# Kernel tuning notes

Measured on AMD Instinct MI355X. Metric: run time of the kernel, lower is better.

## Reference

```python
import jax, jax.numpy as jnp
import numpy as np

NEG = -1e30   # finite stand-in for -inf (keeps vjp NaN-free)
BLANK = 0


def _ctc_loss_mean(logits, targets):
    """CTC loss matching torch.nn.CTCLoss(blank=0, zero_infinity=True,
    reduction='mean') applied to log_softmax(logits).permute(1,0,2), with
    input_lengths = T and uniform target_lengths = L.

    logits:  (B, T, K) raw scores
    targets: (B, L) int labels in [1, K) (no blanks)
    """
    B, T, K = logits.shape
    L = targets.shape[1]
    S = 2 * L + 1  # extended label sequence: blank-interleaved

    logp = jax.nn.log_softmax(logits, axis=-1)  # (B, T, K)

    # extended labels ext = [blank, y1, blank, y2, ..., yL, blank]
    ext = jnp.full((B, S), BLANK, dtype=targets.dtype)
    ext = ext.at[:, 1::2].set(targets)  # (B, S)

    # per-step log-probs of extended labels: lp[b, t, s] = logp[b, t, ext[b, s]]
    lp = jnp.take_along_axis(logp, ext[:, None, :], axis=2)  # (B, T, S)

    # skip transition (s-2 -> s) allowed iff ext[s] != blank and ext[s] != ext[s-2]
    skip = jnp.concatenate(
        [jnp.zeros((B, 2), dtype=bool),
         (ext[:, 2:] != BLANK) & (ext[:, 2:] != ext[:, :-2])], axis=1)  # (B, S)

    # alpha init at t = 0
    alpha0 = jnp.full((B, S), NEG, dtype=logp.dtype)
    alpha0 = alpha0.at[:, 0].set(lp[:, 0, 0]).at[:, 1].set(lp[:, 0, 1])

    pad1 = jnp.full((B, 1), NEG, dtype=logp.dtype)
    pad2 = jnp.full((B, 2), NEG, dtype=logp.dtype)

    def step(alpha, lp_t):
        a1 = alpha                                            # stay
        a2 = jnp.concatenate([pad1, alpha[:, :-1]], axis=1)   # advance 1
        a3 = jnp.concatenate([pad2, alpha[:, :-2]], axis=1)   # advance 2
        a3 = jnp.where(skip, a3, NEG)
        new = jnp.logaddexp(jnp.logaddexp(a1, a2), a3) + lp_t
        return new, None

    xs = jnp.swapaxes(lp[:, 1:, :], 0, 1)  # (T-1, B, S)
    alpha, _ = jax.lax.scan(step, alpha0, xs)

    # total log-likelihood: end at last blank or last label
    logl = jnp.logaddexp(alpha[:, S - 1], alpha[:, S - 2])  # (B,)

    per = -logl / L  # 'mean' reduction divides each loss by target length
    per = jnp.where(logl > -1e29, per, 0.0)  # zero_infinity
    return jnp.mean(per)


def setup_inputs() -> dict:
    key = jax.random.key(0)
    k1, k2 = jax.random.split(key)
    B, T, K, L = 64, 1024, 512, 100
    logits = jax.random.normal(k1, (B, T, K), dtype=jnp.float32)
    targets = jax.random.randint(k2, (B, L), 1, K)  # labels exclude blank=0
    return {"logits": logits, "targets": targets}


def reference(logits, targets):
    return _ctc_loss_mean(logits, targets)
```

## Files before the change

kernel.cpp:

```cpp
#include <hip/hip_runtime.h>
#include <hip/hip_fp16.h>


#define TT 1024
#define BB 64
#define KK 512
#define LL 100
#define DLT 320

static constexpr float L2E = 1.44269504088896340736f;
static constexpr float LN2 = 0.69314718055994530942f;

__device__ __forceinline__ float dpp_shr1_z(float x) {
  return __builtin_bit_cast(float,
      __builtin_amdgcn_update_dpp(0, __builtin_bit_cast(int, x),
                                  0x138, 0xf, 0xf, true));
}
__device__ __forceinline__ int dpp_shr1_zi(int x) {
  return __builtin_amdgcn_update_dpp(0, x, 0x138, 0xf, 0xf, true);
}
__device__ __forceinline__ float slog2(float x) {
  return x > 0.0f ? log2f(x) : -1.0e30f;
}
__device__ __forceinline__ float2 upk(unsigned u) {
  return __half22float2(__builtin_bit_cast(__half2, u));
}

__device__ __forceinline__ void resc(float& S0, float& S1, float& S2,
                                     float& S3, int& ea, float& f1,
                                     float& f2) {
  const float m = fmaxf(fmaxf(S0, S1), fmaxf(S2, S3));
  int E = (int)((__float_as_uint(m) >> 23) & 255) - 127;
  E = (m > 0.0f) ? E : 0;
  const float sc = __uint_as_float((unsigned)(127 - E) << 23);
  S0 *= sc; S1 *= sc; S2 *= sc; S3 *= sc;
  ea += E;
  int dE = dpp_shr1_zi(ea) - ea;
  dE = dE < -250 ? -250 : (dE > 250 ? 250 : dE);
  const int h = dE / 2;
  f1 = __uint_as_float((unsigned)(127 + h) << 23);
  f2 = __uint_as_float((unsigned)(127 + (dE - h)) << 23);
}
__device__ __forceinline__ void refresh_f(int ea, float& f1, float& f2) {
  int dE = dpp_shr1_zi(ea) - ea;
  dE = dE < -250 ? -250 : (dE > 250 ? 250 : dE);
  const int h = dE / 2;
  f1 = __uint_as_float((unsigned)(127 + h) << 23);
  f2 = __uint_as_float((unsigned)(127 + (dE - h)) << 23);
}

__device__ __forceinline__ void fstep(float2 r, float mA, float mB,
                                      float& S0, float& S1, float& S2,
                                      float& S3, float f1, float f2) {
  const float A3 = dpp_shr1_z(S3) * f1 * f2;
  const float n0 = S0 + A3;
  const float n1 = (S0 + S1 + mA * A3) * r.x;
  const float n2 = S1 + S2;
  const float n3 = (S2 + S3 + mB * S1) * r.y;
  S0 = n0; S1 = n1; S2 = n2; S3 = n3;
}
__device__ __forceinline__ void bstep(float2 r, float mBb, float mAn,
                                      float& S0, float& S1, float& S2,
                                      float& S3, float f1, float f2) {
  const float s2 = dpp_shr1_z(r.x);
  const float H0 = dpp_shr1_z(S0) * f1 * f2;
  const float H1 = dpp_shr1_z(S1) * f1 * f2;
  const float u = r.x * S1;
  const float v = r.y * S3;
  const float n0 = S0 + u;
  const float n1 = u + fmaf(mBb, v, S2);
  const float n2 = S2 + v;
  const float n3 = v + fmaf(mAn, s2 * H1, H0);
  S0 = n0; S1 = n1; S2 = n2; S3 = n3;
}

template <int CB, int NC>
__device__ __forceinline__ void run_fwd(const unsigned* __restrict__ gb,
                                        float mA, float mB, float& S0,
                                        float& S1, float& S2, float& S3,
                                        int& ea, float& f1, float& f2) {
  uint2 RA[8], RB[8], RC[8], RD[8];
#define ISSUE(BUF, CHN)                                                    \
  do {                                                                     \
    if ((CHN) < NC) {                                                      \
      _Pragma("unroll") for (int j = 0; j < 8; ++j)                        \
        BUF[j] = *reinterpret_cast<const uint2*>(                          \
            gb + (size_t)((CB + (CHN)) * 8 + j) * 128);                    \
      __builtin_amdgcn_sched_barrier(0);                                   \
    }                                                                      \
  } while (0)
#define COMP(BUF)                                                          \
  do {                                                                     \
    _Pragma("unroll") for (int j = 0; j < 8; ++j) {                        \
      fstep(upk(BUF[j].x), mA, mB, S0, S1, S2, S3, f1, f2);                \
      fstep(upk(BUF[j].y), mA, mB, S0, S1, S2, S3, f1, f2);                \
      if ((j & 3) == 3) resc(S0, S1, S2, S3, ea, f1, f2);                  \
    }                                                                      \
  } while (0)
  ISSUE(RA, 0); ISSUE(RB, 1); ISSUE(RC, 2);
  for (int c = 0; c < NC; c += 4) {
    ISSUE(RD, c + 3); COMP(RA);
    ISSUE(RA, c + 4); COMP(RB);
    ISSUE(RB, c + 5); COMP(RC);
    ISSUE(RC, c + 6); COMP(RD);
  }
#undef ISSUE
#undef COMP
}

template <int CB, int NC>
__device__ __forceinline__ void run_bwd(const unsigned* __restrict__ gb,
                                        float mBb, float mAn, float& S0,
                                        float& S1, float& S2, float& S3,
                                        int& ea, float& f1, float& f2) {
  uint2 RA[8], RB[8], RC[8], RD[8];
#define ISSUE(BUF, CHN)                                                    \
  do {                                                                     \
    if ((CHN) < NC) {                                                      \
      _Pragma("unroll") for (int j = 0; j < 8; ++j)                        \
        BUF[j] = *reinterpret_cast<const uint2*>(                          \
            gb + (size_t)(511 - ((CB + (CHN)) * 8 + j)) * 128);            \
      __builtin_amdgcn_sched_barrier(0);                                   \
    }                                                                      \
  } while (0)
#define COMP(BUF)                                                          \
  do {                                                                     \
    _Pragma("unroll") for (int j = 0; j < 8; ++j) {                        \
      bstep(upk(BUF[j].y), mBb, mAn, S0, S1, S2, S3, f1, f2);              \
      bstep(upk(BUF[j].x), mBb, mAn, S0, S1, S2, S3, f1, f2);              \
      if ((j & 3) == 3) resc(S0, S1, S2, S3, ea, f1, f2);                  \
    }                                                                      \
  } while (0)
  ISSUE(RA, 0); ISSUE(RB, 1); ISSUE(RC, 2);
  for (int c = 0; c < NC; c += 4) {
    ISSUE(RD, c + 3); COMP(RA);
    ISSUE(RA, c + 4); COMP(RB);
    ISSUE(RB, c + 5); COMP(RC);
    ISSUE(RC, c + 6); COMP(RD);
  }
#undef ISSUE
#undef COMP
}

__device__ __forceinline__ void prob_row(const float* __restrict__ logits,
                                         const int* __restrict__ targets,
                                         unsigned* __restrict__ pk,
                                         float* __restrict__ lbArr,
                                         int b, int t, int lane, float* sp) {
  const int row = (b << 10) + t;
  const float* x = logits + (size_t)row * KK;
  const float4 v0 = reinterpret_cast<const float4*>(x)[lane];
  const float4 v1 = reinterpret_cast<const float4*>(x)[lane + 64];
  float4* sp4 = reinterpret_cast<float4*>(sp);
  sp4[lane] = v0;
  sp4[lane + 64] = v1;

  float m = fmaxf(fmaxf(fmaxf(v0.x, v0.y), fmaxf(v0.z, v0.w)),
                  fmaxf(fmaxf(v1.x, v1.y), fmaxf(v1.z, v1.w)));
  #pragma unroll
  for (int d = 1; d < 64; d <<= 1) m = fmaxf(m, __shfl_xor(m, d));

  float e = exp2f((v0.x - m) * L2E) + exp2f((v0.y - m) * L2E) +
            exp2f((v0.z - m) * L2E) + exp2f((v0.w - m) * L2E) +
            exp2f((v1.x - m) * L2E) + exp2f((v1.y - m) * L2E) +
            exp2f((v1.z - m) * L2E) + exp2f((v1.w - m) * L2E);
  #pragma unroll
  for (int d = 1; d < 64; d <<= 1) e += __shfl_xor(e, d);

  __syncthreads();
  const float xb = sp[0];

  float ox = 0.0f, oy = 0.0f;
  if (lane >= 1 && lane <= 50) {
    const int2 c = *reinterpret_cast<const int2*>(
        targets + b * LL + (2 * lane - 2));
    ox = exp2f((sp[c.x] - xb) * L2E);
    oy = exp2f((sp[c.y] - xb) * L2E);
  }
  const int word = (lane == 0) ? 63 : (lane - 1);
  const __half2 h = __floats2half2_rn(ox, oy);
  pk[(size_t)(row >> 1) * 128 + word * 2 + (row & 1)] =
      __builtin_bit_cast(unsigned, h);
  if (lane == 0) lbArr[row] = (xb - m) * L2E + 9.0f - log2f(e);
}

__global__ __launch_bounds__(256) void k_probs_edge(
    const float* __restrict__ logits, const int* __restrict__ targets,
    unsigned* __restrict__ pk, float* __restrict__ lbArr,
    float* __restrict__ out) {
  if (blockIdx.x == 0 && threadIdx.x == 0) out[0] = 0.0f;
  const int wid = threadIdx.x >> 6;
  const int lane = threadIdx.x & 63;
  __shared__ float sx[4][KK];
  const int e = (blockIdx.x << 2) + wid;
  const int b = e / 640;
  const int w = e - b * 640;
  const int t = (w < DLT) ? w : (TT - 640) + w;
  prob_row(logits, targets, pk, lbArr, b, t, lane, sx[wid]);
}

__global__ __launch_bounds__(256) void k_mid(
    const float* __restrict__ logits, const int* __restrict__ targets,
    unsigned* __restrict__ pk, float* __restrict__ lbArr,
    float* __restrict__ st) {
  const int lane = threadIdx.x & 63;
  const int wv = threadIdx.x >> 6;
  __shared__ float sx[4][KK];

  if (blockIdx.x >= BB) {
    const int m = ((blockIdx.x - BB) << 2) + wv;
    const int b = m / 384;
    const int w = m - b * 384;
    prob_row(logits, targets, pk, lbArr, b, DLT + w, lane, sx[wv]);
    return;
  }

  if (wv >= 2) return;
  const int b = blockIdx.x;
  const int dir = wv;
  const int* tg = targets + b * LL;

  float S0 = 0.0f, S1 = 0.0f, S2 = 0.0f, S3 = 0.0f;
  int ea = 0;
  float f1 = 1.0f, f2 = 1.0f;

  if (dir == 0) {
    const unsigned* gb = pk + (size_t)b * 512 * 128 + lane * 2;
    float mA = 0.0f, mB = 0.0f;
    if (lane > 0 && 2 * lane <= LL - 1)
      mA = (tg[2 * lane] != tg[2 * lane - 1]) ? 1.0f : 0.0f;
    if (2 * lane + 1 <= LL - 1)
      mB = (tg[2 * lane + 1] != tg[2 * lane]) ? 1.0f : 0.0f;
    S0 = (lane == 0) ? 1.0f : 0.0f;
    run_fwd<0, 20>(gb, mA, mB, S0, S1, S2, S3, ea, f1, f2);
  } else {
    const int ii = 50 - lane;
    const int w = (ii >= 0) ? ii : 50;
    const unsigned* gb = pk + (size_t)b * 512 * 128 + w * 2;
    float mBb = 0.0f, mAn = 0.0f;
    if (ii >= 0 && 2 * ii + 1 <= LL - 1)
      mBb = (tg[2 * ii + 1] != tg[2 * ii]) ? 1.0f : 0.0f;
    if (ii >= 0 && ii <= 48)
      mAn = (tg[2 * ii + 2] != tg[2 * ii + 1]) ? 1.0f : 0.0f;
    if (lane == 0) S0 = 1.0f;
    if (lane == 1) S3 = 1.0f;
    run_bwd<0, 20>(gb, mBb, mAn, S0, S1, S2, S3, ea, f1, f2);
  }

  float* stp = st + (size_t)(b * 2 + dir) * 5 * 64;
  stp[0 * 64 + lane] = S0;
  stp[1 * 64 + lane] = S1;
  stp[2 * 64 + lane] = S2;
  stp[3 * 64 + lane] = S3;
  stp[4 * 64 + lane] = __int_as_float(ea);
}

__global__ __launch_bounds__(128) void k_tail(
    const unsigned* __restrict__ pk, const float* __restrict__ lbArr,
    const int* __restrict__ targets, const float* __restrict__ st,
    float* __restrict__ out) {
  const int lane = threadIdx.x & 63;
  const int wv = threadIdx.x >> 6;
  const int b = blockIdx.x;
  const int dir = wv;
  const int* tg = targets + b * LL;

  __shared__ float sG[6][64];

  const float4* lbv = reinterpret_cast<const float4*>(lbArr + (size_t)b * TT);
  const int lbbase = (dir == 0) ? 0 : 128;
  const float4 lb0 = lbv[lbbase + lane];
  const float4 lb1 = lbv[lbbase + lane + 64];

  const float* stp = st + (size_t)(b * 2 + dir) * 5 * 64;
  float S0 = stp[0 * 64 + lane];
  float S1 = stp[1 * 64 + lane];
  float S2 = stp[2 * 64 + lane];
  float S3 = stp[3 * 64 + lane];
  int ea = __float_as_int(stp[4 * 64 + lane]);
  float f1, f2;
  refresh_f(ea, f1, f2);

  if (dir == 0) {
    const unsigned* gb = pk + (size_t)b * 512 * 128 + lane * 2;
    float mA = 0.0f, mB = 0.0f;
    if (lane > 0 && 2 * lane <= LL - 1)
      mA = (tg[2 * lane] != tg[2 * lane - 1]) ? 1.0f : 0.0f;
    if (2 * lane + 1 <= LL - 1)
      mB = (tg[2 * lane + 1] != tg[2 * lane]) ? 1.0f : 0.0f;
    run_fwd<20, 12>(gb, mA, mB, S0, S1, S2, S3, ea, f1, f2);
  } else {
    const int ii = 50 - lane;
    const int w = (ii >= 0) ? ii : 50;
    const unsigned* gb = pk + (size_t)b * 512 * 128 + w * 2;
    float mBb = 0.0f, mAn = 0.0f;
    if (ii >= 0 && 2 * ii + 1 <= LL - 1)
      mBb = (tg[2 * ii + 1] != tg[2 * ii]) ? 1.0f : 0.0f;
    if (ii >= 0 && ii <= 48)
      mAn = (tg[2 * ii + 2] != tg[2 * ii + 1]) ? 1.0f : 0.0f;
    run_bwd<20, 12>(gb, mBb, mAn, S0, S1, S2, S3, ea, f1, f2);
  }

  float s4 = (lb0.x + lb0.y) + (lb0.z + lb0.w) +
             (lb1.x + lb1.y) + (lb1.z + lb1.w);
  #pragma unroll
  for (int d = 1; d < 64; d <<= 1) s4 += __shfl_xor(s4, d);

  if (dir == 1) {
    sG[0][lane] = S0; sG[1][lane] = S1; sG[2][lane] = S2; sG[3][lane] = S3;
    sG[4][lane] = (float)ea;
    if (lane == 0) sG[5][0] = s4;
  }
  __syncthreads();

  if (dir == 0) {
    const int gj = (lane <= 50) ? (50 - lane) : 63;
    const float eb = sG[4][gj];
    const float eff = (float)ea;
    float w0 = slog2(S0) + eff + slog2(sG[0][gj]) + eb;
    float w1 = slog2(S1) + eff + slog2(sG[1][gj]) + eb;
    float w2 = slog2(S2) + eff + slog2(sG[2][gj]) + eb;
    float w3 = slog2(S3) + eff + slog2(sG[3][gj]) + eb;
    float wm = fmaxf(fmaxf(w0, w1), fmaxf(w2, w3));
    #pragma unroll
    for (int d = 1; d < 64; d <<= 1) wm = fmaxf(wm, __shfl_xor(wm, d));
    float ss = exp2f(w0 - wm) + exp2f(w1 - wm) +
               exp2f(w2 - wm) + exp2f(w3 - wm);
    #pragma unroll
    for (int d = 1; d < 64; d <<= 1) ss += __shfl_xor(ss, d);

    if (lane == 0) {
      const float lbsum = s4 + sG[5][0];
      float loss = 0.0f;
      if (wm > -1.0e29f) {
        const float logl2 = wm + log2f(ss) + lbsum - (float)(TT * 9);
        loss = -(logl2 * LN2) / (float)LL;
      }
      atomicAdd(out, loss * (1.0f / (float)BB));
    }
  }
}

extern "C" void kernel_launch(void* const* d_in, const int* in_sizes, int n_in,
                              void* d_out, int out_size, void* d_ws, size_t ws_size,
                              hipStream_t stream) {
  const float* logits = (const float*)d_in[0];
  const int* targets = (const int*)d_in[1];
  float* out = (float*)d_out;

  unsigned* pk = (unsigned*)d_ws;
  float* lbArr = (float*)d_ws + (size_t)BB * 512 * 128;
  float* st = lbArr + (size_t)BB * TT;

  hipLaunchKernelGGL(k_probs_edge, dim3(BB * 640 / 4), dim3(256), 0, stream,
                     logits, targets, pk, lbArr, out);
  hipLaunchKernelGGL(k_mid, dim3(BB + BB * 384 / 4), dim3(256), 0, stream,
                     logits, targets, pk, lbArr, st);
  hipLaunchKernelGGL(k_tail, dim3(BB), dim3(128), 0, stream,
                     pk, lbArr, targets, st, out);
}
```

Before: 47.85 us.

## Split pipeline into four stages to overlap more recursion with probability computation

Replaces the three-kernel pipeline (edge probs, mid with recursion plus remaining probs, tail) with four kernels. The forward/backward recursion is now split into chunks of 12, 12 and 8 steps, each running alongside part of the log-softmax row work, so less of the prob work sits alone before the first recursion chunk. Wave max and sum reductions now use DPP row operations plus a readlane in place of shfl_xor butterflies. The cost is one more kernel launch and an extra state round-trip through global memory.

```diff
diff --git a/kernel.cpp b/kernel.cpp
--- a/kernel.cpp
+++ b/kernel.cpp
@@ -6,7 +6,6 @@
 #define BB 64
 #define KK 512
 #define LL 100
-#define DLT 320
 
 static constexpr float L2E = 1.44269504088896340736f;
 static constexpr float LN2 = 0.69314718055994530942f;
@@ -24,6 +23,27 @@
 }
 __device__ __forceinline__ float2 upk(unsigned u) {
   return __half22float2(__builtin_bit_cast(__half2, u));
+}
+
+__device__ __forceinline__ float wave_max_dpp(float v) {
+#define DPPMAX(C)                                                          \
+  v = fmaxf(v, __builtin_bit_cast(float, __builtin_amdgcn_update_dpp(      \
+                   0, __builtin_bit_cast(int, v), C, 0xf, 0xf, true)))
+  DPPMAX(0x111); DPPMAX(0x112); DPPMAX(0x114); DPPMAX(0x118);
+  DPPMAX(0x142); DPPMAX(0x143);
+#undef DPPMAX
+  return __builtin_bit_cast(float,
+      __builtin_amdgcn_readlane(__builtin_bit_cast(int, v), 63));
+}
+__device__ __forceinline__ float wave_sum_dpp(float v) {
+#define DPPADD(C)                                                          \
+  v = v + __builtin_bit_cast(float, __builtin_amdgcn_update_dpp(           \
+              0, __builtin_bit_cast(int, v), C, 0xf, 0xf, true))
+  DPPADD(0x111); DPPADD(0x112); DPPADD(0x114); DPPADD(0x118);
+  DPPADD(0x142); DPPADD(0x143);
+#undef DPPADD
+  return __builtin_bit_cast(float,
+      __builtin_amdgcn_readlane(__builtin_bit_cast(int, v), 63));
 }
 
 __device__ __forceinline__ void resc(float& S0, float& S1, float& S2,
@@ -157,15 +177,13 @@
 
   float m = fmaxf(fmaxf(fmaxf(v0.x, v0.y), fmaxf(v0.z, v0.w)),
                   fmaxf(fmaxf(v1.x, v1.y), fmaxf(v1.z, v1.w)));
-  #pragma unroll
-  for (int d = 1; d < 64; d <<= 1) m = fmaxf(m, __shfl_xor(m, d));
+  m = wave_max_dpp(m);
 
   float e = exp2f((v0.x - m) * L2E) + exp2f((v0.y - m) * L2E) +
             exp2f((v0.z - m) * L2E) + exp2f((v0.w - m) * L2E) +
             exp2f((v1.x - m) * L2E) + exp2f((v1.y - m) * L2E) +
             exp2f((v1.z - m) * L2E) + exp2f((v1.w - m) * L2E);
-  #pragma unroll
-  for (int d = 1; d < 64; d <<= 1) e += __shfl_xor(e, d);
+  e = wave_sum_dpp(e);
 
   __syncthreads();
   const float xb = sp[0];
@@ -184,37 +202,56 @@
   if (lane == 0) lbArr[row] = (xb - m) * L2E + 9.0f - log2f(e);
 }
 
-__global__ __launch_bounds__(256) void k_probs_edge(
+__device__ __forceinline__ void fwd_masks(const int* tg, int lane,
+                                          float& mA, float& mB) {
+  mA = 0.0f; mB = 0.0f;
+  if (lane > 0 && 2 * lane <= LL - 1)
+    mA = (tg[2 * lane] != tg[2 * lane - 1]) ? 1.0f : 0.0f;
+  if (2 * lane + 1 <= LL - 1)
+    mB = (tg[2 * lane + 1] != tg[2 * lane]) ? 1.0f : 0.0f;
+}
+__device__ __forceinline__ void bwd_masks(const int* tg, int lane,
+                                          float& mBb, float& mAn, int& w) {
+  const int ii = 50 - lane;
+  w = (ii >= 0) ? ii : 50;
+  mBb = 0.0f; mAn = 0.0f;
+  if (ii >= 0 && 2 * ii + 1 <= LL - 1)
+    mBb = (tg[2 * ii + 1] != tg[2 * ii]) ? 1.0f : 0.0f;
+  if (ii >= 0 && ii <= 48)
+    mAn = (tg[2 * ii + 2] != tg[2 * ii + 1]) ? 1.0f : 0.0f;
+}
+
+__global__ __launch_bounds__(256) void k_p1(
     const float* __restrict__ logits, const int* __restrict__ targets,
     unsigned* __restrict__ pk, float* __restrict__ lbArr,
     float* __restrict__ out) {
   if (blockIdx.x == 0 && threadIdx.x == 0) out[0] = 0.0f;
-  const int wid = threadIdx.x >> 6;
+  const int wv = threadIdx.x >> 6;
   const int lane = threadIdx.x & 63;
   __shared__ float sx[4][KK];
-  const int e = (blockIdx.x << 2) + wid;
-  const int b = e / 640;
-  const int w = e - b * 640;
-  const int t = (w < DLT) ? w : (TT - 640) + w;
-  prob_row(logits, targets, pk, lbArr, b, t, lane, sx[wid]);
-}
-
-__global__ __launch_bounds__(256) void k_mid(
+  const int e = (blockIdx.x << 2) + wv;
+  const int b = e / 384;
+  const int w = e - b * 384;
+  const int t = (w < 192) ? w : (w + 640);
+  prob_row(logits, targets, pk, lbArr, b, t, lane, sx[wv]);
+}
+
+__global__ __launch_bounds__(256) void k_mid1(
     const float* __restrict__ logits, const int* __restrict__ targets,
     unsigned* __restrict__ pk, float* __restrict__ lbArr,
-    float* __restrict__ st) {
+    float* __restrict__ st1) {
   const int lane = threadIdx.x & 63;
   const int wv = threadIdx.x >> 6;
   __shared__ float sx[4][KK];
 
   if (blockIdx.x >= BB) {
-    const int m = ((blockIdx.x - BB) << 2) + wv;
-    const int b = m / 384;
-    const int w = m - b * 384;
-    prob_row(logits, targets, pk, lbArr, b, DLT + w, lane, sx[wv]);
+    const int e = ((blockIdx.x - BB) << 2) + wv;
+    const int b = e / 384;
+    const int w = e - b * 384;
+    const int t = (w < 192) ? (w + 192) : (w + 448);
+    prob_row(logits, targets, pk, lbArr, b, t, lane, sx[wv]);
     return;
   }
-
   if (wv >= 2) return;
   const int b = blockIdx.x;
   const int dir = wv;
@@ -226,28 +263,19 @@
 
   if (dir == 0) {
     const unsigned* gb = pk + (size_t)b * 512 * 128 + lane * 2;
-    float mA = 0.0f, mB = 0.0f;
-    if (lane > 0 && 2 * lane <= LL - 1)
-      mA = (tg[2 * lane] != tg[2 * lane - 1]) ? 1.0f : 0.0f;
-    if (2 * lane + 1 <= LL - 1)
-      mB = (tg[2 * lane + 1] != tg[2 * lane]) ? 1.0f : 0.0f;
+    float mA, mB;
+    fwd_masks(tg, lane, mA, mB);
     S0 = (lane == 0) ? 1.0f : 0.0f;
-    run_fwd<0, 20>(gb, mA, mB, S0, S1, S2, S3, ea, f1, f2);
+    run_fwd<0, 12>(gb, mA, mB, S0, S1, S2, S3, ea, f1, f2);
   } else {
-    const int ii = 50 - lane;
-    const int w = (ii >= 0) ? ii : 50;
+    float mBb, mAn; int w;
+    bwd_masks(tg, lane, mBb, mAn, w);
     const unsigned* gb = pk + (size_t)b * 512 * 128 + w * 2;
-    float mBb = 0.0f, mAn = 0.0f;
-    if (ii >= 0 && 2 * ii + 1 <= LL - 1)
-      mBb = (tg[2 * ii + 1] != tg[2 * ii]) ? 1.0f : 0.0f;
-    if (ii >= 0 && ii <= 48)
-      mAn = (tg[2 * ii + 2] != tg[2 * ii + 1]) ? 1.0f : 0.0f;
     if (lane == 0) S0 = 1.0f;
     if (lane == 1) S3 = 1.0f;
-    run_bwd<0, 20>(gb, mBb, mAn, S0, S1, S2, S3, ea, f1, f2);
-  }
-
-  float* stp = st + (size_t)(b * 2 + dir) * 5 * 64;
+    run_bwd<0, 12>(gb, mBb, mAn, S0, S1, S2, S3, ea, f1, f2);
+  }
+  float* stp = st1 + (size_t)(b * 2 + dir) * 5 * 64;
   stp[0 * 64 + lane] = S0;
   stp[1 * 64 + lane] = S1;
   stp[2 * 64 + lane] = S2;
@@ -255,9 +283,57 @@
   stp[4 * 64 + lane] = __int_as_float(ea);
 }
 
+__global__ __launch_bounds__(256) void k_mid2(
+    const float* __restrict__ logits, const int* __restrict__ targets,
+    unsigned* __restrict__ pk, float* __restrict__ lbArr,
+    const float* __restrict__ st1, float* __restrict__ st2) {
+  const int lane = threadIdx.x & 63;
+  const int wv = threadIdx.x >> 6;
+  __shared__ float sx[4][KK];
+
+  if (blockIdx.x >= BB) {
+    const int e = ((blockIdx.x - BB) << 2) + wv;
+    const int b = e >> 8;
+    const int w = e & 255;
+    prob_row(logits, targets, pk, lbArr, b, 384 + w, lane, sx[wv]);
+    return;
+  }
+  if (wv >= 2) return;
+  const int b = blockIdx.x;
+  const int dir = wv;
+  const int* tg = targets + b * LL;
+
+  const float* sp = st1 + (size_t)(b * 2 + dir) * 5 * 64;
+  float S0 = sp[0 * 64 + lane];
+  float S1 = sp[1 * 64 + lane];
+  float S2 = sp[2 * 64 + lane];
+  float S3 = sp[3 * 64 + lane];
+  int ea = __float_as_int(sp[4 * 64 + lane]);
+  float f1, f2;
+  refresh_f(ea, f1, f2);
+
+  if (dir == 0) {
+    const unsigned* gb = pk + (size_t)b * 512 * 128 + lane * 2;
+    float mA, mB;
+    fwd_masks(tg, lane, mA, mB);
+    run_fwd<12, 12>(gb, mA, mB, S0, S1, S2, S3, ea, f1, f2);
+  } else {
+    float mBb, mAn; int w;
+    bwd_masks(tg, lane, mBb, mAn, w);
+    const unsigned* gb = pk + (size_t)b * 512 * 128 + w * 2;
+    run_bwd<12, 12>(gb, mBb, mAn, S0, S1, S2, S3, ea, f1, f2);
+  }
+  float* stp = st2 + (size_t)(b * 2 + dir) * 5 * 64;
+  stp[0 * 64 + lane] = S0;
+  stp[1 * 64 + lane] = S1;
+  stp[2 * 64 + lane] = S2;
+  stp[3 * 64 + lane] = S3;
+  stp[4 * 64 + lane] = __int_as_float(ea);
+}
+
 __global__ __launch_bounds__(128) void k_tail(
     const unsigned* __restrict__ pk, const float* __restrict__ lbArr,
-    const int* __restrict__ targets, const float* __restrict__ st,
+    const int* __restrict__ targets, const float* __restrict__ st2,
     float* __restrict__ out) {
   const int lane = threadIdx.x & 63;
   const int wv = threadIdx.x >> 6;
@@ -272,33 +348,25 @@
   const float4 lb0 = lbv[lbbase + lane];
   const float4 lb1 = lbv[lbbase + lane + 64];
 
-  const float* stp = st + (size_t)(b * 2 + dir) * 5 * 64;
-  float S0 = stp[0 * 64 + lane];
-  float S1 = stp[1 * 64 + lane];
-  float S2 = stp[2 * 64 + lane];
-  float S3 = stp[3 * 64 + lane];
-  int ea = __float_as_int(stp[4 * 64 + lane]);
+  const float* sp = st2 + (size_t)(b * 2 + dir) * 5 * 64;
+  float S0 = sp[0 * 64 + lane];
+  float S1 = sp[1 * 64 + lane];
+  float S2 = sp[2 * 64 + lane];
+  float S3 = sp[3 * 64 + lane];
+  int ea = __float_as_int(sp[4 * 64 + lane]);
   float f1, f2;
   refresh_f(ea, f1, f2);
 
   if (dir == 0) {
     const unsigned* gb = pk + (size_t)b * 512 * 128 + lane * 2;
-    float mA = 0.0f, mB = 0.0f;
-    if (lane > 0 && 2 * lane <= LL - 1)
-      mA = (tg[2 * lane] != tg[2 * lane - 1]) ? 1.0f : 0.0f;
-    if (2 * lane + 1 <= LL - 1)
-      mB = (tg[2 * lane + 1] != tg[2 * lane]) ? 1.0f : 0.0f;
-    run_fwd<20, 12>(gb, mA, mB, S0, S1, S2, S3, ea, f1, f2);
+    float mA, mB;
+    fwd_masks(tg, lane, mA, mB);
+    run_fwd<24, 8>(gb, mA, mB, S0, S1, S2, S3, ea, f1, f2);
   } else {
-    const int ii = 50 - lane;
-    const int w = (ii >= 0) ? ii : 50;
+    float mBb, mAn; int w;
+    bwd_masks(tg, lane, mBb, mAn, w);
     const unsigned* gb = pk + (size_t)b * 512 * 128 + w * 2;
-    float mBb = 0.0f, mAn = 0.0f;
-    if (ii >= 0 && 2 * ii + 1 <= LL - 1)
-      mBb = (tg[2 * ii + 1] != tg[2 * ii]) ? 1.0f : 0.0f;
-    if (ii >= 0 && ii <= 48)
-      mAn = (tg[2 * ii + 2] != tg[2 * ii + 1]) ? 1.0f : 0.0f;
-    run_bwd<20, 12>(gb, mBb, mAn, S0, S1, S2, S3, ea, f1, f2);
+    run_bwd<24, 8>(gb, mBb, mAn, S0, S1, S2, S3, ea, f1, f2);
   }
 
   float s4 = (lb0.x + lb0.y) + (lb0.z + lb0.w) +
@@ -350,12 +418,15 @@
 
   unsigned* pk = (unsigned*)d_ws;
   float* lbArr = (float*)d_ws + (size_t)BB * 512 * 128;
-  float* st = lbArr + (size_t)BB * TT;
-
-  hipLaunchKernelGGL(k_probs_edge, dim3(BB * 640 / 4), dim3(256), 0, stream,
+  float* st1 = lbArr + (size_t)BB * TT;
+  float* st2 = st1 + (size_t)BB * 2 * 5 * 64;
+
+  hipLaunchKernelGGL(k_p1, dim3(BB * 384 / 4), dim3(256), 0, stream,
                      logits, targets, pk, lbArr, out);
-  hipLaunchKernelGGL(k_mid, dim3(BB + BB * 384 / 4), dim3(256), 0, stream,
-                     logits, targets, pk, lbArr, st);
+  hipLaunchKernelGGL(k_mid1, dim3(BB + BB * 384 / 4), dim3(256), 0, stream,
+                     logits, targets, pk, lbArr, st1);
+  hipLaunchKernelGGL(k_mid2, dim3(BB + BB * 256 / 4), dim3(256), 0, stream,
+                     logits, targets, pk, lbArr, st1, st2);
   hipLaunchKernelGGL(k_tail, dim3(BB), dim3(128), 0, stream,
-                     pk, lbArr, targets, st, out);
-}
+                     pk, lbArr, targets, st2, out);
+}
```

Measured after the change: 48.46 us. About the same (+1.3%).
